# Performance work log

Measured on AMD Instinct MI355X. Metric: run time of the kernel, lower is better.

## Reference

```python
import jax, jax.numpy as jnp
import numpy as np

TEMP = 0.5
EPS = 1e-12  # matches torch F.normalize default eps


def _l2_normalize(x):
    n = jnp.sqrt(jnp.sum(x * x, axis=1, keepdims=True))
    return x / jnp.maximum(n, EPS)


def setup_inputs() -> dict:
    key = jax.random.key(0)
    k1, k2 = jax.random.split(key)
    B, D = 4096, 256
    return {
        "x_i": jax.random.normal(k1, (B, D), dtype=jnp.float32),
        "x_j": jax.random.normal(k2, (B, D), dtype=jnp.float32),
    }


def reference(x_i, x_j):
    B = x_i.shape[0]
    z = jnp.concatenate([_l2_normalize(x_i), _l2_normalize(x_j)], axis=0)  # [2B, D]
    # cosine similarity of normalized vectors == plain matmul
    sim = z @ z.T  # [2B, 2B]
    pos = jnp.concatenate([jnp.diagonal(sim, B), jnp.diagonal(sim, -B)], axis=0)  # [2B]
    neg_mask = 1.0 - jnp.eye(2 * B, dtype=sim.dtype)
    denom = jnp.sum(neg_mask * jnp.exp(sim / TEMP), axis=1)  # [2B]
    # -log(exp(pos/T) / denom) = -pos/T + log(denom)
    loss = jnp.sum(-(pos / TEMP) + jnp.log(denom)) / (2 * B)
    return loss
```

## Files before the change

kernel.cpp:

```cpp
#include <hip/hip_runtime.h>
#include <hip/hip_bf16.h>

#define B_ROWS 4096
#define NROWS  8192
#define D      256
#define NPANEL 32
#define NSEG   32
#define NBLK2  512
#define TT     264

typedef __attribute__((ext_vector_type(8))) short bf16x8;
typedef __attribute__((ext_vector_type(4))) float floatx4;

__global__ __launch_bounds__(256) void norm_pos_kernel(
    const float* __restrict__ xi, const float* __restrict__ xj,
    short* __restrict__ z, float* __restrict__ pos,
    float* __restrict__ selfdot, float* __restrict__ rowsum,
    float* __restrict__ out, unsigned int* __restrict__ counter) {
    int gt = blockIdx.x * 256 + threadIdx.x;
    if (gt < NROWS) rowsum[gt] = 0.f;
    if (gt == 0) { out[0] = 0.f; counter[0] = 0u; }

    int p    = blockIdx.x * 4 + (threadIdx.x >> 6);
    int lane = threadIdx.x & 63;
    float4 v1 = ((const float4*)(xi + (size_t)p * D))[lane];
    float4 v2 = ((const float4*)(xj + (size_t)p * D))[lane];
    float ss1 = v1.x * v1.x + v1.y * v1.y + v1.z * v1.z + v1.w * v1.w;
    float ss2 = v2.x * v2.x + v2.y * v2.y + v2.z * v2.z + v2.w * v2.w;
#pragma unroll
    for (int off = 32; off > 0; off >>= 1) {
        ss1 += __shfl_xor(ss1, off);
        ss2 += __shfl_xor(ss2, off);
    }
    float sc1 = 1.0f / fmaxf(sqrtf(ss1), 1e-12f);
    float sc2 = 1.0f / fmaxf(sqrtf(ss2), 1e-12f);

    union { __hip_bfloat16 h[4]; short4 s4; } u1, u2;
    u1.h[0] = __float2bfloat16(v1.x * sc1); u1.h[1] = __float2bfloat16(v1.y * sc1);
    u1.h[2] = __float2bfloat16(v1.z * sc1); u1.h[3] = __float2bfloat16(v1.w * sc1);
    u2.h[0] = __float2bfloat16(v2.x * sc2); u2.h[1] = __float2bfloat16(v2.y * sc2);
    u2.h[2] = __float2bfloat16(v2.z * sc2); u2.h[3] = __float2bfloat16(v2.w * sc2);
    ((short4*)(z + (size_t)p * D))[lane]            = u1.s4;
    ((short4*)(z + (size_t)(p + B_ROWS) * D))[lane] = u2.s4;

    float sd1 = 0.f, sd2 = 0.f, dp = 0.f;
#pragma unroll
    for (int j = 0; j < 4; j++) {
        float a = __bfloat162float(u1.h[j]);
        float b = __bfloat162float(u2.h[j]);
        sd1 += a * a; sd2 += b * b; dp += a * b;
    }
#pragma unroll
    for (int off = 32; off > 0; off >>= 1) {
        sd1 += __shfl_xor(sd1, off);
        sd2 += __shfl_xor(sd2, off);
        dp  += __shfl_xor(dp,  off);
    }
    if (lane == 0) {
        pos[p] = dp; pos[p + B_ROWS] = dp;
        selfdot[p] = sd1; selfdot[p + B_ROWS] = sd2;
    }
}

__global__ __launch_bounds__(256, 2) void sim_rowsum_kernel(
    const short* __restrict__ z, float* __restrict__ rowsum,
    const float* __restrict__ pos, const float* __restrict__ selfdot,
    unsigned int* __restrict__ counter, float* __restrict__ out) {
    __shared__ __align__(16) short Bbuf[2][8192];
    __shared__ unsigned int done_s;
    __shared__ float sdata[4];

    const int tid  = threadIdx.x;
    const int lane = tid & 63;
    const int w    = tid >> 6;
    const int lm   = lane & 15;
    const int lg   = lane >> 4;

    const int s  = blockIdx.x >> 5;
    const int q  = blockIdx.x & 31;
    const int L0 = 256 - 8 * s;
    const int cb = (q * TT) >> 5;
    const int ce = ((q + 1) * TT) >> 5;

    const int scol = tid >> 3;
    const int sg   = tid & 7;
    const int sxor = scol & 7;

    const int fxor = lm & 7;

    bf16x8 a[8][4];
    floatx4 acc[4][2];
    float rsacc[4][4];
    bf16x8 pf[4];

#pragma unroll
    for (int mi = 0; mi < 4; mi++)
#pragma unroll
        for (int r = 0; r < 4; r++) rsacc[mi][r] = 0.f;

    auto decode = [&](int c, int& panel, int& colbase, bool& mirror) {
        int cloc;
        if (c < L0) { panel = s;      cloc = c; }
        else        { panel = 31 - s; cloc = c - L0; }
        colbase = panel * 256 + cloc * 32;
        mirror  = (cloc >= 8);
    };

    auto loadA = [&](int panel) {
#pragma unroll
        for (int kk = 0; kk < 8; kk++)
#pragma unroll
            for (int mi = 0; mi < 4; mi++)
                a[kk][mi] = *(const bf16x8*)(
                    z + (size_t)(panel * 256 + w * 64 + mi * 16 + lm) * D +
                    kk * 32 + lg * 8);
    };

    auto flushRs = [&](int panel) {
#pragma unroll
        for (int mi = 0; mi < 4; mi++)
#pragma unroll
            for (int r = 0; r < 4; r++) {
                float v = rsacc[mi][r];
                v += __shfl_xor(v, 1); v += __shfl_xor(v, 2);
                v += __shfl_xor(v, 4); v += __shfl_xor(v, 8);
                if (lm == 0)
                    atomicAdd(&rowsum[panel * 256 + w * 64 + mi * 16 + lg * 4 + r], v);
                rsacc[mi][r] = 0.f;
            }
    };

    auto fetch = [&](int colbase) {
        const short* p = z + (size_t)(colbase + scol) * D + sg * 8;
#pragma unroll
        for (int j = 0; j < 4; j++) pf[j] = *(const bf16x8*)(p + j * 64);
    };
    auto writeB = [&](int buf) {
#pragma unroll
        for (int j = 0; j < 4; j++) {
            int u = scol * 32 + ((sg + 8 * j) ^ sxor);
            *(bf16x8*)(&Bbuf[buf][u * 8]) = pf[j];
        }
    };

    int panel, colbase; bool mirror;
    decode(cb, panel, colbase, mirror);
    int curpanel = panel;
    fetch(colbase);
    writeB(0);
    loadA(panel);
    __syncthreads();

    for (int c = cb; c < ce; c++) {
        const int buf = (c - cb) & 1;
        decode(c, panel, colbase, mirror);

        const bool hn = (c + 1 < ce);
        if (hn) {
            int npanel, ncolbase; bool nm;
            decode(c + 1, npanel, ncolbase, nm);
            fetch(ncolbase);
        }
        if (panel != curpanel) {
            flushRs(curpanel);
            loadA(panel);
            curpanel = panel;
        }

#pragma unroll
        for (int mi = 0; mi < 4; mi++)
#pragma unroll
            for (int ni = 0; ni < 2; ni++)
                acc[mi][ni] = (floatx4){0.f, 0.f, 0.f, 0.f};

#pragma unroll
        for (int kk = 0; kk < 8; kk++) {
            bf16x8 b0 = *(const bf16x8*)(
                &Bbuf[buf][(( (0 * 16 + lm) * 32) + ((kk * 4 + lg) ^ fxor)) * 8]);
            bf16x8 b1 = *(const bf16x8*)(
                &Bbuf[buf][(( (1 * 16 + lm) * 32) + ((kk * 4 + lg) ^ fxor)) * 8]);
#pragma unroll
            for (int mi = 0; mi < 4; mi++)
                acc[mi][0] = __builtin_amdgcn_mfma_f32_16x16x32_bf16(
                    a[kk][mi], b0, acc[mi][0], 0, 0, 0);
#pragma unroll
            for (int mi = 0; mi < 4; mi++)
                acc[mi][1] = __builtin_amdgcn_mfma_f32_16x16x32_bf16(
                    a[kk][mi], b1, acc[mi][1], 0, 0, 0);
        }

        float cs0 = 0.f, cs1 = 0.f;
#pragma unroll
        for (int mi = 0; mi < 4; mi++)
#pragma unroll
            for (int r = 0; r < 4; r++) {
                float e0 = __expf(2.0f * acc[mi][0][r]);
                float e1 = __expf(2.0f * acc[mi][1][r]);
                rsacc[mi][r] += e0 + e1;
                cs0 += e0; cs1 += e1;
            }
        if (mirror) {
            cs0 += __shfl_xor(cs0, 16); cs0 += __shfl_xor(cs0, 32);
            cs1 += __shfl_xor(cs1, 16); cs1 += __shfl_xor(cs1, 32);
            if (lane < 16) {
                atomicAdd(&rowsum[colbase + lane],      cs0);
                atomicAdd(&rowsum[colbase + 16 + lane], cs1);
            }
        }

        if (hn) {
            writeB(buf ^ 1);
            __syncthreads();
        }
    }
    flushRs(curpanel);

    __syncthreads();
    if (tid == 0) {
        __threadfence();
        done_s = atomicAdd(counter, 1u);
    }
    __syncthreads();
    if (done_s == (unsigned int)(NBLK2 - 1)) {
        __threadfence();
        float acc_l = 0.f;
#pragma unroll 4
        for (int r = tid; r < NROWS; r += 256) {
            float rsv = __hip_atomic_load(&rowsum[r], __ATOMIC_RELAXED,
                                          __HIP_MEMORY_SCOPE_AGENT);
            float denom = rsv - __expf(2.0f * selfdot[r]);
            acc_l += -2.0f * pos[r] + logf(denom);
        }
#pragma unroll
        for (int off = 32; off > 0; off >>= 1) acc_l += __shfl_xor(acc_l, off);
        if (lane == 0) sdata[w] = acc_l;
        __syncthreads();
        if (tid == 0)
            out[0] = (sdata[0] + sdata[1] + sdata[2] + sdata[3]) / (float)NROWS;
    }
}

extern "C" void kernel_launch(void* const* d_in, const int* in_sizes, int n_in,
                              void* d_out, int out_size, void* d_ws, size_t ws_size,
                              hipStream_t stream) {
    const float* xi = (const float*)d_in[0];
    const float* xj = (const float*)d_in[1];
    float* out      = (float*)d_out;

    char* ws        = (char*)d_ws;
    short* z        = (short*)ws;
    float* rowsum   = (float*)(ws + (size_t)NROWS * D * 2);
    float* pos      = rowsum + NROWS;
    float* selfdot  = pos + NROWS;
    unsigned int* counter = (unsigned int*)(selfdot + NROWS);

    norm_pos_kernel<<<B_ROWS / 4, 256, 0, stream>>>(xi, xj, z, pos, selfdot,
                                                    rowsum, out, counter);
    sim_rowsum_kernel<<<NBLK2, 256, 0, stream>>>(z, rowsum, pos, selfdot,
                                                 counter, out);
}
```

Measured before the change: 100.8 us.

## Split row panels across two blocks and stage B via global_load_lds

Each block now covers 128 rows of the panel instead of 256, doubling the grid to 1024 blocks and halving A-fragment register use so launch bounds can request 4 blocks per CU. The B column tile is loaded directly into LDS with global_load_lds (swizzled addressing), replacing register prefetch plus a separate LDS write. This aims to raise occupancy and cut register pressure and staging instructions. In exchange, B tiles are fetched twice as often overall, there are more rowsum atomics per column in the mirror path, and a sync now runs on every iteration.

Result: slower. 113.7 us (+12.9%).

```diff
diff --git a/kernel.cpp b/kernel.cpp
--- a/kernel.cpp
+++ b/kernel.cpp
@@ -4,10 +4,8 @@
 #define B_ROWS 4096
 #define NROWS  8192
 #define D      256
-#define NPANEL 32
-#define NSEG   32
-#define NBLK2  512
 #define TT     264
+#define NBLK2  1024
 
 typedef __attribute__((ext_vector_type(8))) short bf16x8;
 typedef __attribute__((ext_vector_type(4))) float floatx4;
@@ -62,7 +60,7 @@
     }
 }
 
-__global__ __launch_bounds__(256, 2) void sim_rowsum_kernel(
+__global__ __launch_bounds__(256, 4) void sim_rowsum_kernel(
     const short* __restrict__ z, float* __restrict__ rowsum,
     const float* __restrict__ pos, const float* __restrict__ selfdot,
     unsigned int* __restrict__ counter, float* __restrict__ out) {
@@ -75,26 +73,22 @@
     const int w    = tid >> 6;
     const int lm   = lane & 15;
     const int lg   = lane >> 4;
-
-    const int s  = blockIdx.x >> 5;
-    const int q  = blockIdx.x & 31;
-    const int L0 = 256 - 8 * s;
-    const int cb = (q * TT) >> 5;
-    const int ce = ((q + 1) * TT) >> 5;
-
-    const int scol = tid >> 3;
-    const int sg   = tid & 7;
-    const int sxor = scol & 7;
-
     const int fxor = lm & 7;
 
-    bf16x8 a[8][4];
-    floatx4 acc[4][2];
-    float rsacc[4][4];
-    bf16x8 pf[4];
-
-#pragma unroll
-    for (int mi = 0; mi < 4; mi++)
+    const int bid = blockIdx.x;
+    const int s   = bid >> 6;
+    const int q   = (bid >> 1) & 31;
+    const int h   = bid & 1;
+    const int L0  = 256 - 8 * s;
+    const int cb  = (q * TT) >> 5;
+    const int ce  = ((q + 1) * TT) >> 5;
+
+    bf16x8 a[8][2];
+    floatx4 acc[2][2];
+    float rsacc[2][4];
+
+#pragma unroll
+    for (int mi = 0; mi < 2; mi++)
 #pragma unroll
         for (int r = 0; r < 4; r++) rsacc[mi][r] = 0.f;
 
@@ -106,48 +100,56 @@
         mirror  = (cloc >= 8);
     };
 
+    auto decodeCol = [&](int c) {
+        int cloc, panel;
+        if (c < L0) { panel = s;      cloc = c; }
+        else        { panel = 31 - s; cloc = c - L0; }
+        return panel * 256 + cloc * 32;
+    };
+
     auto loadA = [&](int panel) {
 #pragma unroll
         for (int kk = 0; kk < 8; kk++)
 #pragma unroll
-            for (int mi = 0; mi < 4; mi++)
+            for (int mi = 0; mi < 2; mi++)
                 a[kk][mi] = *(const bf16x8*)(
-                    z + (size_t)(panel * 256 + w * 64 + mi * 16 + lm) * D +
+                    z + (size_t)(panel * 256 + h * 128 + w * 32 + mi * 16 + lm) * D +
                     kk * 32 + lg * 8);
     };
 
     auto flushRs = [&](int panel) {
 #pragma unroll
-        for (int mi = 0; mi < 4; mi++)
+        for (int mi = 0; mi < 2; mi++)
 #pragma unroll
             for (int r = 0; r < 4; r++) {
                 float v = rsacc[mi][r];
                 v += __shfl_xor(v, 1); v += __shfl_xor(v, 2);
                 v += __shfl_xor(v, 4); v += __shfl_xor(v, 8);
                 if (lm == 0)
-                    atomicAdd(&rowsum[panel * 256 + w * 64 + mi * 16 + lg * 4 + r], v);
+                    atomicAdd(&rowsum[panel * 256 + h * 128 + w * 32 + mi * 16 +
+                                      lg * 4 + r], v);
                 rsacc[mi][r] = 0.f;
             }
     };
 
-    auto fetch = [&](int colbase) {
-        const short* p = z + (size_t)(colbase + scol) * D + sg * 8;
-#pragma unroll
-        for (int j = 0; j < 4; j++) pf[j] = *(const bf16x8*)(p + j * 64);
-    };
-    auto writeB = [&](int buf) {
+    auto stage = [&](int buf, int colbase) {
 #pragma unroll
         for (int j = 0; j < 4; j++) {
-            int u = scol * 32 + ((sg + 8 * j) ^ sxor);
-            *(bf16x8*)(&Bbuf[buf][u * 8]) = pf[j];
+            int col = w * 8 + j * 2 + (lane >> 5);
+            int c16 = (lane & 31) ^ (col & 7);
+            const short* src = z + (size_t)(colbase + col) * D + c16 * 8;
+            __builtin_amdgcn_global_load_lds(
+                (const __attribute__((address_space(1))) unsigned int*)src,
+                (__attribute__((address_space(3))) unsigned int*)
+                    &Bbuf[buf][(w * 4 + j) * 512],
+                16, 0, 0);
         }
     };
 
     int panel, colbase; bool mirror;
     decode(cb, panel, colbase, mirror);
     int curpanel = panel;
-    fetch(colbase);
-    writeB(0);
+    stage(0, colbase);
     loadA(panel);
     __syncthreads();
 
@@ -155,12 +157,9 @@
         const int buf = (c - cb) & 1;
         decode(c, panel, colbase, mirror);
 
-        const bool hn = (c + 1 < ce);
-        if (hn) {
-            int npanel, ncolbase; bool nm;
-            decode(c + 1, npanel, ncolbase, nm);
-            fetch(ncolbase);
-        }
+        if (c + 1 < ce)
+            stage(buf ^ 1, decodeCol(c + 1));
+
         if (panel != curpanel) {
             flushRs(curpanel);
             loadA(panel);
@@ -168,7 +167,7 @@
         }
 
 #pragma unroll
-        for (int mi = 0; mi < 4; mi++)
+        for (int mi = 0; mi < 2; mi++)
 #pragma unroll
             for (int ni = 0; ni < 2; ni++)
                 acc[mi][ni] = (floatx4){0.f, 0.f, 0.f, 0.f};
@@ -176,22 +175,22 @@
 #pragma unroll
         for (int kk = 0; kk < 8; kk++) {
             bf16x8 b0 = *(const bf16x8*)(
-                &Bbuf[buf][(( (0 * 16 + lm) * 32) + ((kk * 4 + lg) ^ fxor)) * 8]);
+                &Bbuf[buf][((lm) * 32 + ((kk * 4 + lg) ^ fxor)) * 8]);
             bf16x8 b1 = *(const bf16x8*)(
-                &Bbuf[buf][(( (1 * 16 + lm) * 32) + ((kk * 4 + lg) ^ fxor)) * 8]);
-#pragma unroll
-            for (int mi = 0; mi < 4; mi++)
-                acc[mi][0] = __builtin_amdgcn_mfma_f32_16x16x32_bf16(
-                    a[kk][mi], b0, acc[mi][0], 0, 0, 0);
-#pragma unroll
-            for (int mi = 0; mi < 4; mi++)
-                acc[mi][1] = __builtin_amdgcn_mfma_f32_16x16x32_bf16(
-                    a[kk][mi], b1, acc[mi][1], 0, 0, 0);
+                &Bbuf[buf][((16 + lm) * 32 + ((kk * 4 + lg) ^ fxor)) * 8]);
+            acc[0][0] = __builtin_amdgcn_mfma_f32_16x16x32_bf16(
+                a[kk][0], b0, acc[0][0], 0, 0, 0);
+            acc[1][0] = __builtin_amdgcn_mfma_f32_16x16x32_bf16(
+                a[kk][1], b0, acc[1][0], 0, 0, 0);
+            acc[0][1] = __builtin_amdgcn_mfma_f32_16x16x32_bf16(
+                a[kk][0], b1, acc[0][1], 0, 0, 0);
+            acc[1][1] = __builtin_amdgcn_mfma_f32_16x16x32_bf16(
+                a[kk][1], b1, acc[1][1], 0, 0, 0);
         }
 
         float cs0 = 0.f, cs1 = 0.f;
 #pragma unroll
-        for (int mi = 0; mi < 4; mi++)
+        for (int mi = 0; mi < 2; mi++)
 #pragma unroll
             for (int r = 0; r < 4; r++) {
                 float e0 = __expf(2.0f * acc[mi][0][r]);
@@ -208,10 +207,7 @@
             }
         }
 
-        if (hn) {
-            writeB(buf ^ 1);
-            __syncthreads();
-        }
+        __syncthreads();
     }
     flushRs(curpanel);
 
```

## Load B tiles directly from global memory instead of via double-buffered LDS

Applied to the files above, without the earlier changes.

Removes the shared-memory double buffer, the cooperative prefetch into LDS, and the per-iteration block barrier. Each wave now reads its B fragments directly from global memory, relying on L1/L2 caching since all four waves read the same 32 columns. This drops the LDS footprint and sync overhead, but each wave issues redundant global loads and software prefetch overlap is lost, which may expose load latency before the MFMAs.

New measurement: 118.9 us. 1.18x slower.

```diff
diff --git a/kernel.cpp b/kernel.cpp
--- a/kernel.cpp
+++ b/kernel.cpp
@@ -4,10 +4,8 @@
 #define B_ROWS 4096
 #define NROWS  8192
 #define D      256
-#define NPANEL 32
-#define NSEG   32
+#define TT     264
 #define NBLK2  512
-#define TT     264
 
 typedef __attribute__((ext_vector_type(8))) short bf16x8;
 typedef __attribute__((ext_vector_type(4))) float floatx4;
@@ -66,7 +64,6 @@
     const short* __restrict__ z, float* __restrict__ rowsum,
     const float* __restrict__ pos, const float* __restrict__ selfdot,
     unsigned int* __restrict__ counter, float* __restrict__ out) {
-    __shared__ __align__(16) short Bbuf[2][8192];
     __shared__ unsigned int done_s;
     __shared__ float sdata[4];
 
@@ -76,22 +73,15 @@
     const int lm   = lane & 15;
     const int lg   = lane >> 4;
 
-    const int s  = blockIdx.x >> 5;
-    const int q  = blockIdx.x & 31;
-    const int L0 = 256 - 8 * s;
-    const int cb = (q * TT) >> 5;
-    const int ce = ((q + 1) * TT) >> 5;
-
-    const int scol = tid >> 3;
-    const int sg   = tid & 7;
-    const int sxor = scol & 7;
-
-    const int fxor = lm & 7;
+    const int s   = blockIdx.x >> 5;
+    const int q   = blockIdx.x & 31;
+    const int L0  = 256 - 8 * s;
+    const int cb  = (q * TT) >> 5;
+    const int ce  = ((q + 1) * TT) >> 5;
 
     bf16x8 a[8][4];
     floatx4 acc[4][2];
     float rsacc[4][4];
-    bf16x8 pf[4];
 
 #pragma unroll
     for (int mi = 0; mi < 4; mi++)
@@ -130,37 +120,14 @@
             }
     };
 
-    auto fetch = [&](int colbase) {
-        const short* p = z + (size_t)(colbase + scol) * D + sg * 8;
-#pragma unroll
-        for (int j = 0; j < 4; j++) pf[j] = *(const bf16x8*)(p + j * 64);
-    };
-    auto writeB = [&](int buf) {
-#pragma unroll
-        for (int j = 0; j < 4; j++) {
-            int u = scol * 32 + ((sg + 8 * j) ^ sxor);
-            *(bf16x8*)(&Bbuf[buf][u * 8]) = pf[j];
-        }
-    };
-
     int panel, colbase; bool mirror;
     decode(cb, panel, colbase, mirror);
     int curpanel = panel;
-    fetch(colbase);
-    writeB(0);
     loadA(panel);
-    __syncthreads();
 
     for (int c = cb; c < ce; c++) {
-        const int buf = (c - cb) & 1;
         decode(c, panel, colbase, mirror);
 
-        const bool hn = (c + 1 < ce);
-        if (hn) {
-            int npanel, ncolbase; bool nm;
-            decode(c + 1, npanel, ncolbase, nm);
-            fetch(ncolbase);
-        }
         if (panel != curpanel) {
             flushRs(curpanel);
             loadA(panel);
@@ -173,12 +140,13 @@
             for (int ni = 0; ni < 2; ni++)
                 acc[mi][ni] = (floatx4){0.f, 0.f, 0.f, 0.f};
 
+        const short* bbase = z + (size_t)colbase * D;
 #pragma unroll
         for (int kk = 0; kk < 8; kk++) {
             bf16x8 b0 = *(const bf16x8*)(
-                &Bbuf[buf][(( (0 * 16 + lm) * 32) + ((kk * 4 + lg) ^ fxor)) * 8]);
+                bbase + (size_t)lm * D + kk * 32 + lg * 8);
             bf16x8 b1 = *(const bf16x8*)(
-                &Bbuf[buf][(( (1 * 16 + lm) * 32) + ((kk * 4 + lg) ^ fxor)) * 8]);
+                bbase + (size_t)(16 + lm) * D + kk * 32 + lg * 8);
 #pragma unroll
             for (int mi = 0; mi < 4; mi++)
                 acc[mi][0] = __builtin_amdgcn_mfma_f32_16x16x32_bf16(
@@ -207,11 +175,6 @@
                 atomicAdd(&rowsum[colbase + 16 + lane], cs1);
             }
         }
-
-        if (hn) {
-            writeB(buf ^ 1);
-            __syncthreads();
-        }
     }
     flushRs(curpanel);
 
```
